# Optimization experiments

Hardware: AMD Instinct MI355X
Metric: run time of the kernel (lower is better)

## Reference

```python
import jax, jax.numpy as jnp
import numpy as np

IMC = 256
EPS = 1e-6
BN_EPS = 1e-5
GRID = (69.12, 79.36)      # (depth, width) in meters
OFF = (0.0, -39.68, 0.0)   # (xoff, yoff, zoff)
RES = 0.64
ZMIN, ZMAX = -3.0, 2.76
SCALES = [0.25, 0.125, 0.0625, 0.03125, 0.015625]


def make_corners():
    # replicates make_grid(): corner lattice in lidar coords, shape [nz, nx, ny, 3]
    nx = int(round(GRID[0] / RES)) + 1   # 109
    ny = int(round(GRID[1] / RES)) + 1   # 125
    nz = int(round((ZMAX - ZMIN) / RES)) + 1  # 10
    xc = RES * np.arange(nx) + OFF[0]
    yc = GRID[1] - RES * np.arange(ny) + OFF[1]
    zc = ZMAX - RES * np.arange(nz)
    xx, yy = np.meshgrid(xc, yc, indexing='ij')
    base = np.stack([xx, yy, np.full_like(xx, OFF[2])], axis=-1)  # [nx,ny,3]
    zoffs = np.stack([np.zeros(nz), np.zeros(nz), zc], axis=-1)   # [nz,3]
    corners = base[None] + zoffs[:, None, None, :]
    return jnp.asarray(corners, jnp.float32)


def grid_sample(img, grid):
    # img [B,C,H,W]; grid [B,P,N,2] xy in [-1,1]; bilinear, zero padding, align_corners=False
    B, C, H, W = img.shape
    x = (grid[..., 0] + 1.0) * (W * 0.5) - 0.5
    y = (grid[..., 1] + 1.0) * (H * 0.5) - 0.5
    x0f = jnp.floor(x); y0f = jnp.floor(y)
    wx = (x - x0f).reshape(B, 1, -1)
    wy = (y - y0f).reshape(B, 1, -1)
    x0 = x0f.astype(jnp.int32); y0 = y0f.astype(jnp.int32)
    flat = img.reshape(B, C, H * W)
    def g(xi, yi):
        ok = ((xi >= 0) & (xi < W) & (yi >= 0) & (yi < H)).reshape(B, 1, -1)
        idx = (jnp.clip(yi, 0, H - 1) * W + jnp.clip(xi, 0, W - 1)).reshape(B, 1, -1)
        return jnp.take_along_axis(flat, idx, axis=2) * ok
    v00 = g(x0, y0); v01 = g(x0 + 1, y0); v10 = g(x0, y0 + 1); v11 = g(x0 + 1, y0 + 1)
    out = (v00 * (1 - wx) + v01 * wx) * (1 - wy) + (v10 * (1 - wx) + v11 * wx) * wy
    return out.reshape(B, C, grid.shape[1], grid.shape[2])


def oft(feats, calib, corners, scale, w, b):
    B, C, Hf, Wf = feats.shape
    # perspective projection of grid corners into the image plane
    hom = jnp.einsum('bij,zdwj->bzdwi', calib[:, :, :3], corners) + calib[:, None, None, None, :, 3]
    xy = hom[..., :2] / hom[..., 2:3]                      # [B,nz,nx,ny,2]
    img_size = jnp.array([Wf, Hf], jnp.float32) / scale
    nc = jnp.clip(2.0 * xy / img_size - 1.0, -1.0, 1.0)
    mn = jnp.minimum(nc[:, :-1, :-1, :-1], nc[:, :-1, 1:, :-1])
    mx = jnp.maximum(nc[:, 1:, 1:, 1:], nc[:, 1:, :-1, 1:])
    bbox = jnp.concatenate([mn, mx], axis=-1)              # [B,Zc,Dc,Wc,4]
    _, Zc, Dc, Wc, _ = bbox.shape
    bbox = bbox.reshape(B, Zc, Dc * Wc, 4)
    area = ((bbox[..., 2] - bbox[..., 0]) * (bbox[..., 3] - bbox[..., 1])
            * (Hf * Wf * 0.25) + EPS)[:, None]             # [B,1,Zc,N]
    visible = (area > EPS).astype(feats.dtype)
    ii = jnp.cumsum(jnp.cumsum(feats, axis=-1), axis=-2)   # integral image
    tl = grid_sample(ii, jnp.stack([bbox[..., 0], bbox[..., 1]], -1))
    br = grid_sample(ii, jnp.stack([bbox[..., 2], bbox[..., 3]], -1))
    tr = grid_sample(ii, jnp.stack([bbox[..., 2], bbox[..., 1]], -1))
    bl = grid_sample(ii, jnp.stack([bbox[..., 0], bbox[..., 3]], -1))
    vox = (tl + br - tr - bl) / area * visible             # [B,C,Zc,N]
    vox = vox.transpose(0, 3, 1, 2).reshape(B * Dc * Wc, C * Zc)
    ortho = jax.nn.relu(vox @ w.T + b).reshape(B, Dc, Wc, -1)
    return ortho.transpose(0, 3, 2, 1)                     # [B,imc,Wc,Dc]


def attention(x, aw, ab):
    s = jax.nn.sigmoid(x.mean(axis=(2, 3)) @ aw.T + ab)
    return x * s[:, :, None, None]


def conv3x3(x, w, stride):
    return jax.lax.conv_general_dilated(x, w, (stride, stride), ((1, 1), (1, 1)),
                                        dimension_numbers=('NCHW', 'OIHW', 'NCHW'))


def bn(x, g, b, m, v):
    scale = g / jnp.sqrt(v + BN_EPS)
    return (x - m[None, :, None, None]) * scale[None, :, None, None] + b[None, :, None, None]


def make_calib(B):
    K = np.array([[560.0, 0.0, 640.0], [0.0, 560.0, 192.0], [0.0, 0.0, 1.0]])
    Rt = np.array([[0.0, -1.0, 0.0, 0.05],   # lidar(x fwd, y left, z up) -> cam(x right, y down, z fwd)
                   [0.0, 0.0, -1.0, -0.30],
                   [1.0, 0.0, 0.0, 0.27]])
    P = K @ Rt
    return jnp.asarray(np.tile(P[None], (B, 1, 1)), jnp.float32)


def setup_inputs() -> dict:
    key = jax.random.key(0)
    ks = jax.random.split(key, 16)
    B = 1
    shapes = [(B, IMC, 96, 320), (B, IMC, 48, 160), (B, IMC, 24, 80), (B, IMC, 12, 40), (B, IMC, 6, 20)]
    feats = [jax.random.normal(ks[i], s, jnp.float32) * 0.1 for i, s in enumerate(shapes)]
    HC = 9 * IMC  # height_channels = int((2.76-(-3))/0.64 * 256) = 2304
    inp = {
        'feats04': feats[0], 'feats08': feats[1], 'feats16': feats[2],
        'feats32': feats[3], 'feats64': feats[4],
        'calib': make_calib(B),
        'oft_w': jax.random.normal(ks[5], (5, IMC, HC), jnp.float32) * 0.02,
        'oft_b': jax.random.normal(ks[6], (5, IMC), jnp.float32) * 0.02,
        'att_w': jax.random.normal(ks[7], (IMC, IMC), jnp.float32) * 0.05,
        'att_b': jnp.zeros((IMC,), jnp.float32),
        'conv1_w': jax.random.normal(ks[8], (IMC, IMC * 5, 3, 3), jnp.float32) * 0.02,
        'bn1_g': 1.0 + 0.1 * jax.random.normal(ks[9], (IMC,), jnp.float32),
        'bn1_b': 0.05 * jax.random.normal(ks[10], (IMC,), jnp.float32),
        'bn1_m': 0.05 * jax.random.normal(ks[11], (IMC,), jnp.float32),
        'bn1_v': jax.random.uniform(ks[12], (IMC,), jnp.float32, 0.5, 1.5),
        'conv2_w': jax.random.normal(ks[13], (IMC, IMC, 3, 3), jnp.float32) * 0.02,
        'bn2_g': 1.0 + 0.1 * jax.random.normal(ks[14], (IMC,), jnp.float32),
        'bn2_b': jnp.zeros((IMC,), jnp.float32),
        'bn2_m': jnp.zeros((IMC,), jnp.float32),
        'bn2_v': jax.random.uniform(ks[15], (IMC,), jnp.float32, 0.5, 1.5),
    }
    return inp


def reference(feats04, feats08, feats16, feats32, feats64, calib,
              oft_w, oft_b, att_w, att_b,
              conv1_w, bn1_g, bn1_b, bn1_m, bn1_v,
              conv2_w, bn2_g, bn2_b, bn2_m, bn2_v):
    corners = make_corners()
    feats = [feats04, feats08, feats16, feats32, feats64]
    orthos = [attention(oft(f, calib, corners, s, oft_w[i], oft_b[i]), att_w, att_b)
              for i, (f, s) in enumerate(zip(feats, SCALES))]
    x = jnp.concatenate(orthos, axis=1)            # [B, 5*imc, 124, 108]
    x = jax.nn.relu(bn(conv3x3(x, conv1_w, 2), bn1_g, bn1_b, bn1_m, bn1_v))
    x = jax.nn.relu(bn(conv3x3(x, conv2_w, 1), bn2_g, bn2_b, bn2_m, bn2_v))
    return x                                       # [B, imc, 62, 54]
```

## Files before the change

kernel.cpp:

```cpp
#include <hip/hip_runtime.h>

typedef __attribute__((ext_vector_type(8))) short short8;
typedef __attribute__((ext_vector_type(4))) float float4v;
typedef __attribute__((ext_vector_type(4))) int int4v;
typedef __attribute__((ext_vector_type(4))) unsigned short ushort4v;

#define NBOX 13392
#define ZC 9
#define KOFT 2304
#define NPIX 3348
#define NBLK0 105
#define NBLKC 27
#define TILEK 4096
#define NBSTRIDE 294912
#define VOXSZ 30965760
#define TAPINTS 16

__device__ __forceinline__ unsigned short f2bf(float f) {
  union { float f; unsigned int i; } v; v.f = f;
  unsigned int r = v.i + 0x7FFFu + ((v.i >> 16) & 1u);
  return (unsigned short)(r >> 16);
}
__device__ __forceinline__ float bf2f(unsigned short u) {
  union { unsigned int i; float f; } v; v.i = ((unsigned int)u) << 16; return v.f;
}
__device__ __forceinline__ float i2f(int i) {
  union { int i; float f; } v; v.i = i; return v.f;
}

__device__ __constant__ int cHFs[5] = {96, 48, 24, 12, 6};
__device__ __constant__ int cWFs[5] = {320, 160, 80, 40, 20};
__device__ __constant__ size_t cIIof[5] = {0, 7864320, 9830400, 10321920, 10444800};

__device__ __forceinline__ const int* uniform_ptr(const int* p) {
  unsigned lo = (unsigned)(uintptr_t)p;
  unsigned hi = (unsigned)((uintptr_t)p >> 32);
  lo = (unsigned)__builtin_amdgcn_readfirstlane((int)lo);
  hi = (unsigned)__builtin_amdgcn_readfirstlane((int)hi);
  return (const int*)(((uintptr_t)hi << 32) | (uintptr_t)lo);
}

__device__ __forceinline__ void async16(const unsigned short* g, unsigned short* l) {
  __builtin_amdgcn_global_load_lds(
      (const __attribute__((address_space(1))) unsigned int*)g,
      (__attribute__((address_space(3))) unsigned int*)l, 16, 0, 0);
}

__global__ void k_alpha_beta(const float* __restrict__ oft_b,
                             const float* __restrict__ g1, const float* __restrict__ b1,
                             const float* __restrict__ m1, const float* __restrict__ v1,
                             const float* __restrict__ g2, const float* __restrict__ b2,
                             const float* __restrict__ m2, const float* __restrict__ v2,
                             float* __restrict__ ALPHA, float* __restrict__ BETA,
                             float* __restrict__ MEANS, unsigned short* __restrict__ ZPAGE) {
  int g = blockIdx.x, c = threadIdx.x;
  float al, be;
  if (g < 5) { al = 1.f; be = oft_b[g * 256 + c]; MEANS[g * 256 + c] = 0.f; }
  else {
    const float* gg = (g == 5) ? g1 : g2;
    const float* bb = (g == 5) ? b1 : b2;
    const float* mm = (g == 5) ? m1 : m2;
    const float* vv = (g == 5) ? v1 : v2;
    al = gg[c] / sqrtf(vv[c] + 1e-5f);
    be = bb[c] - mm[c] * al;
  }
  ALPHA[g * 256 + c] = al; BETA[g * 256 + c] = be;
  if (g == 0) ZPAGE[c] = 0;
}

__global__ void k_wpermT(const float* __restrict__ w, unsigned short* __restrict__ wp) {
  int b = blockIdx.x;
  int sc = b >> 8, oc = b & 255;
  int t = threadIdx.x;
  const float* src = w + (size_t)b * 2304;
  int row = oc & 127, cb = oc >> 7;
  unsigned short* dst = wp + (size_t)sc * 589824 + (size_t)cb * 294912 + row * 8;
#pragma unroll
  for (int i = 0; i < 9; ++i) {
    int idx = i * 256 + t;
    float v = src[idx];
    int c = idx / 9, z = idx - c * 9;
    int k = z * 256 + c;
    int s = k >> 5, kc = (k >> 3) & 3, j = k & 7;
    dst[(size_t)s * 4096 + kc * 1024 + j] = f2bf(v);
  }
}

__global__ void k_wperm1T(const float* __restrict__ w, const float* __restrict__ satt,
                          unsigned short* __restrict__ wp) {
  int oc = blockIdx.x;
  int t = threadIdx.x;
  const float* src = w + (size_t)oc * 11520;
  int row = oc & 127, cb = oc >> 7;
  unsigned short* dst = wp + (size_t)cb * (9 * 40 * 4096) + row * 8;
#pragma unroll
  for (int i = 0; i < 45; ++i) {
    int idx = i * 256 + t;
    float v = src[idx];
    int ic = idx / 9, r = idx - ic * 9;
    int s = ic >> 5, kc = (ic >> 3) & 3, j = ic & 7;
    dst[(size_t)(r * 40 + s) * 4096 + kc * 1024 + j] = f2bf(v * satt[ic]);
  }
}

__global__ void k_wperm2T(const float* __restrict__ w, unsigned short* __restrict__ wp) {
  int oc = blockIdx.x;
  int t = threadIdx.x;
  const float* src = w + (size_t)oc * 2304;
  int row = oc & 127, cb = oc >> 7;
  unsigned short* dst = wp + (size_t)cb * (9 * 8 * 4096) + row * 8;
#pragma unroll
  for (int i = 0; i < 9; ++i) {
    int idx = i * 256 + t;
    float v = src[idx];
    int ic = idx / 9, r = idx - ic * 9;
    int s = ic >> 5, kc = (ic >> 3) & 3, j = ic & 7;
    dst[(size_t)(r * 8 + s) * 4096 + kc * 1024 + j] = f2bf(v);
  }
}

__global__ void k_tapsA(const float* __restrict__ calib, int* __restrict__ taps, int s0) {
  int idx = blockIdx.x * 256 + threadIdx.x;
  if (idx >= ZC * NBOX) return;
  int slab = blockIdx.y, sc = s0 + slab;
  int Hf = cHFs[sc], Wf = cWFs[sc];
  float areaScale = (float)(Hf * Wf) * 0.25f;
  int z = idx / NBOX, n = idx % NBOX;
  int d = n / 124, wj = n % 124;
  float P[12];
#pragma unroll
  for (int i = 0; i < 12; ++i) P[i] = calib[i];
  auto proj = [&](int k, int i, int j, float& nxo, float& nyo) {
    float X = 0.64f * (float)i;
    float Y = 39.68f - 0.64f * (float)j;
    float Z = 2.76f - 0.64f * (float)k;
    float hx = P[0] * X + P[1] * Y + P[2]  * Z + P[3];
    float hy = P[4] * X + P[5] * Y + P[6]  * Z + P[7];
    float hz = P[8] * X + P[9] * Y + P[10] * Z + P[11];
    float px = hx / hz, py = hy / hz;
    nxo = 2.f * px / 1280.f - 1.f; nxo = fminf(fmaxf(nxo, -1.f), 1.f);
    nyo = 2.f * py / 384.f  - 1.f; nyo = fminf(fmaxf(nyo, -1.f), 1.f);
  };
  float ax, ay, bx, by, cx, cy, dx, dy;
  proj(z,     d,     wj,     ax, ay);
  proj(z,     d + 1, wj,     bx, by);
  proj(z + 1, d + 1, wj + 1, cx, cy);
  proj(z + 1, d,     wj + 1, dx, dy);
  float x0 = fminf(ax, bx), y0 = fminf(ay, by);
  float x1 = fmaxf(cx, dx), y1 = fmaxf(cy, dy);
  float rawA = (x1 - x0) * (y1 - y0) * areaScale;
  int* ob = taps + (size_t)slab * (ZC * NBOX * TAPINTS) + (size_t)idx * TAPINTS;
  if (!(rawA > 0.f)) { ob[0] = 0; return; }
  float inv = 1.f / (rawA + 1e-6f);

  float u0 = (x0 + 1.f) * ((float)Wf * 0.5f) - 0.5f;
  float u1 = (x1 + 1.f) * ((float)Wf * 0.5f) - 0.5f;
  float fu0 = floorf(u0), fu1 = floorf(u1);
  int cx0 = (int)fu0, cx1 = (int)fu1;
  float wx0 = u0 - fu0, wx1 = u1 - fu1;
  int xs[4]; float xw[4];
  xs[0] = cx0; xs[1] = cx0 + 1; xs[2] = cx1; xs[3] = cx1 + 1;
  xw[0] = (1.f - wx0) * inv; xw[1] = wx0 * inv;
  xw[2] = -(1.f - wx1) * inv; xw[3] = -wx1 * inv;
  int dcx = cx1 - cx0;
  if (dcx == 0)      { xw[0] += xw[2]; xw[1] += xw[3]; xw[2] = 0.f; xw[3] = 0.f; }
  else if (dcx == 1) { xw[1] += xw[2]; xw[2] = xw[3]; xs[2] = xs[3]; xw[3] = 0.f; }
#pragma unroll
  for (int j = 0; j < 4; ++j) {
    if (xs[j] < 0 || xs[j] >= Wf) xw[j] = 0.f;
    xs[j] = min(max(xs[j], 0), Wf - 1);
  }
#define CSWX(a, b) { if (xw[a] == 0.f && xw[b] != 0.f) { \
    float tw = xw[a]; xw[a] = xw[b]; xw[b] = tw; \
    int ts = xs[a]; xs[a] = xs[b]; xs[b] = ts; } }
  CSWX(0, 1) CSWX(2, 3) CSWX(0, 2) CSWX(1, 3) CSWX(1, 2)
#undef CSWX
  int nx = (xw[0] != 0.f) + (xw[1] != 0.f) + (xw[2] != 0.f) + (xw[3] != 0.f);

  float v0 = (y0 + 1.f) * ((float)Hf * 0.5f) - 0.5f;
  float v1 = (y1 + 1.f) * ((float)Hf * 0.5f) - 0.5f;
  float fv0 = floorf(v0), fv1 = floorf(v1);
  int ry0 = (int)fv0, ry1 = (int)fv1;
  float wy0 = v0 - fv0, wy1 = v1 - fv1;
  int ys[4]; float yw[4];
  ys[0] = ry0; ys[1] = ry0 + 1; ys[2] = ry1; ys[3] = ry1 + 1;
  yw[0] = 1.f - wy0; yw[1] = wy0; yw[2] = -(1.f - wy1); yw[3] = -wy1;
  int dcy = ry1 - ry0;
  if (dcy == 0)      { yw[0] += yw[2]; yw[1] += yw[3]; yw[2] = 0.f; yw[3] = 0.f; }
  else if (dcy == 1) { yw[1] += yw[2]; yw[2] = yw[3]; ys[2] = ys[3]; yw[3] = 0.f; }
#pragma unroll
  for (int j = 0; j < 4; ++j) {
    if (ys[j] < 0 || ys[j] >= Hf) yw[j] = 0.f;
    ys[j] = min(max(ys[j], 0), Hf - 1);
  }
#define CSWY(a, b) { if (yw[a] == 0.f && yw[b] != 0.f) { \
    float tw = yw[a]; yw[a] = yw[b]; yw[b] = tw; \
    int ts = ys[a]; ys[a] = ys[b]; ys[b] = ts; } }
  CSWY(0, 1) CSWY(2, 3) CSWY(0, 2) CSWY(1, 3) CSWY(1, 2)
#undef CSWY
  int ny = (yw[0] != 0.f) + (yw[1] != 0.f) + (yw[2] != 0.f) + (yw[3] != 0.f);

  if (nx == 0 || ny == 0) { ob[0] = 0; return; }

  int4v* obv = (int4v*)ob;
  obv[0] = (int4v){(xs[0] << 10) | (nx << 25) | (ny << 28),
                   xs[1] << 10, xs[2] << 10, xs[3] << 10};
  obv[1] = (int4v){ys[0] * Wf * 1024, ys[1] * Wf * 1024,
                   ys[2] * Wf * 1024, ys[3] * Wf * 1024};
  float4v* wb = (float4v*)ob;
  wb[2] = (float4v){xw[0], xw[1], xw[2], xw[3]};
  wb[3] = (float4v){yw[0], yw[1], yw[2], yw[3]};
}

__global__ void k_transpose_all(const float* __restrict__ f0, const float* __restrict__ f1,
                                const float* __restrict__ f2, const float* __restrict__ f3,
                                const float* __restrict__ f4, float* __restrict__ II) {
  int b = blockIdx.x;
  int sc, cx;
  if (b < 480)      { sc = 0; cx = b; }
  else if (b < 600) { sc = 1; cx = b - 480; }
  else if (b < 630) { sc = 2; cx = b - 600; }
  else if (b < 638) { sc = 3; cx = b - 630; }
  else              { sc = 4; cx = b - 638; }
  const int Ss[5] = {30720, 7680, 1920, 480, 120};
  const float* srcs[5] = {f0, f1, f2, f3, f4};
  int S = Ss[sc];
  const float* src = srcs[sc];
  float* dst = II + cIIof[sc];
  __shared__ float tile[64][65];
  int t = threadIdx.x;
  int wave = t >> 6, lane = t & 63;
  int s0 = cx * 64, c0 = blockIdx.y * 64;
#pragma unroll
  for (int i = 0; i < 16; ++i) {
    int c_l = wave * 16 + i;
    if (s0 + lane < S) tile[c_l][lane] = src[(size_t)(c0 + c_l) * S + s0 + lane];
  }
  __syncthreads();
#pragma unroll
  for (int i = 0; i < 16; ++i) {
    int s_l = wave * 16 + i;
    if (s0 + s_l < S) dst[(size_t)(s0 + s_l) * 256 + c0 + lane] = tile[lane][s_l];
  }
}

__global__ void k_cumw_all(float* __restrict__ II) {
  int b = blockIdx.x;
  int sc, h;
  if (b < 96)       { sc = 0; h = b; }
  else if (b < 144) { sc = 1; h = b - 96; }
  else if (b < 168) { sc = 2; h = b - 144; }
  else if (b < 180) { sc = 3; h = b - 168; }
  else              { sc = 4; h = b - 180; }
  int Wf = cWFs[sc];
  float* p = II + cIIof[sc] + (size_t)h * Wf * 256 + threadIdx.x;
  float acc = 0.f;
#pragma unroll 4
  for (int w = 0; w < Wf; ++w) { acc += p[(size_t)w * 256]; p[(size_t)w * 256] = acc; }
}

__global__ void k_cumh_all(float* __restrict__ II) {
  int b = blockIdx.x;
  int sc, w;
  if (b < 320)      { sc = 0; w = b; }
  else if (b < 480) { sc = 1; w = b - 320; }
  else if (b < 560) { sc = 2; w = b - 480; }
  else if (b < 600) { sc = 3; w = b - 560; }
  else              { sc = 4; w = b - 600; }
  const int Hfs[5] = {96, 48, 24, 12, 6};
  int Hf = Hfs[sc];
  size_t stride = (size_t)cWFs[sc] * 256;
  float* p = II + cIIof[sc] + (size_t)w * 256 + threadIdx.x;
  float acc = 0.f;
#pragma unroll 4
  for (int h = 0; h < Hf; ++h) { acc += p[h * stride]; p[h * stride] = acc; }
}

__global__ __launch_bounds__(512) void k_sampleA(const float* __restrict__ II,
                                                 const int* __restrict__ taps,
                                                 unsigned short* __restrict__ voxT,
                                                 int s0) {
  __shared__ unsigned short st[3][8][66][4];
  int t = threadIdx.x;
  int wave = t >> 6, lane = t & 63;
  int n = blockIdx.x * 8 + wave;
  int zg = blockIdx.y * 3;
  int slab = blockIdx.z, sc = s0 + slab;
  const float* ii = II + cIIof[sc];
  const int* tbase = taps + (size_t)slab * (ZC * NBOX * TAPINTS);
  unsigned short* vox = voxT + (size_t)slab * VOXSZ;
  const char* iib = (const char*)ii + (lane << 4);
#pragma unroll
  for (int dz = 0; dz < 3; ++dz) {
    int z = zg + dz;
    const int* tb = uniform_ptr(tbase + (size_t)(z * NBOX + n) * TAPINTS);
    int xo[4], yo[4]; float xw[4], yw[4];
#pragma unroll
    for (int i = 0; i < 4; ++i) xo[i] = tb[i];
#pragma unroll
    for (int i = 0; i < 4; ++i) yo[i] = tb[4 + i];
#pragma unroll
    for (int i = 0; i < 4; ++i) xw[i] = i2f(tb[8 + i]);
#pragma unroll
    for (int i = 0; i < 4; ++i) yw[i] = i2f(tb[12 + i]);
    unsigned h = (unsigned)xo[0];
    int nx = (h >> 25) & 7;
    int ny = (h >> 28) & 7;
    xo[0] = (int)(h & 0x01FFFFFFu);
    ushort4v o;
    if (ny == 0) {
      o[0] = 0; o[1] = 0; o[2] = 0; o[3] = 0;
    } else {
      int o_[16]; float w_[16];
#pragma unroll
      for (int r = 0; r < 4; ++r)
#pragma unroll
        for (int c = 0; c < 4; ++c) {
          o_[r * 4 + c] = yo[r] + xo[c];
          w_[r * 4 + c] = yw[r] * xw[c];
        }
      float4v a0 = {0.f, 0.f, 0.f, 0.f}, a1 = a0;
#define TAP(i, acc) { float4v t_ = *(const float4v*)(iib + (size_t)(unsigned)o_[i]); acc += t_ * w_[i]; }
      TAP(0, a0)
      if (nx > 1) TAP(1, a1)
      if (nx > 2) TAP(2, a0)
      if (nx > 3) TAP(3, a1)
      if (ny > 1) {
        TAP(4, a0)
        if (nx > 1) TAP(5, a1)
        if (nx > 2) TAP(6, a0)
        if (nx > 3) TAP(7, a1)
      }
      if (ny > 2) {
        TAP(8, a0)
        if (nx > 1) TAP(9, a1)
        if (nx > 2) TAP(10, a0)
        if (nx > 3) TAP(11, a1)
      }
      if (ny > 3) {
        TAP(12, a0)
        if (nx > 1) TAP(13, a1)
        if (nx > 2) TAP(14, a0)
        if (nx > 3) TAP(15, a1)
      }
#undef TAP
      float4v acc = a0 + a1;
#pragma unroll
      for (int j = 0; j < 4; ++j) o[j] = f2bf(acc[j]);
    }
    *(ushort4v*)&st[dz][wave][lane][0] = o;
  }
  __syncthreads();
  int nb = (blockIdx.x * 8) >> 7;
  int r0 = (blockIdx.x * 8) & 127;
  unsigned short* outb = vox + (size_t)nb * NBSTRIDE + (size_t)r0 * 32;
  int lane32 = t & 31;
  int row = lane32 >> 2, kc = lane32 & 3;
#pragma unroll
  for (int p = 0; p < 2; ++p) {
    int q = p * 16 + (t >> 5);
    if (q < 24) {
      int zq = q >> 3;
      int si = q & 7;
      short8 v = *(const short8*)&st[zq][row][si * 8 + kc * 2][0];
      *(short8*)(outb + (size_t)(zg + zq) * 32768 + (size_t)si * 4096
                 + (size_t)(row * 32 + kc * 8)) = v;
    }
  }
}

__global__ __launch_bounds__(512) void k_gemmT_all(
    const unsigned short* __restrict__ AT, const unsigned short* __restrict__ BT,
    const float* __restrict__ beta, unsigned short* __restrict__ xbuf,
    float* __restrict__ means, int s0) {
  __shared__ unsigned short ls[8704];
  __shared__ float lsm[128];
  unsigned short* lsA = ls;
  unsigned short* lsB = ls + 4096;
  int t = threadIdx.x;
  int lane = t & 63, wave = t >> 6;
  int l15 = lane & 15, quad = lane >> 4;
  int nb = blockIdx.x, cb = blockIdx.y;
  int slab = blockIdx.z, sc = s0 + slab;
  int wrow = (wave & 3) * 32, wcol = (wave >> 2) * 64;

  const unsigned short* ga = AT + (size_t)slab * VOXSZ + (size_t)nb * NBSTRIDE + t * 8;
  const unsigned short* gb = BT + (size_t)sc * 589824 + (size_t)cb * NBSTRIDE + t * 8;
  unsigned short* ldA = lsA + t * 8;
  unsigned short* ldB = lsB + t * 8;

  float4v acc[2][4];
#pragma unroll
  for (int mi = 0; mi < 2; ++mi)
#pragma unroll
    for (int ni = 0; ni < 4; ++ni) acc[mi][ni] = (float4v){0.f, 0.f, 0.f, 0.f};

  for (int s = 0; s < 72; ++s) {
    async16(ga, ldA);
    async16(gb, ldB);
    ga += TILEK; gb += TILEK;
    __syncthreads();
    short8 af[2], bf[4];
    const short8* pA = (const short8*)lsA;
    const short8* pB = (const short8*)lsB;
#pragma unroll
    for (int mi = 0; mi < 2; ++mi) af[mi] = pA[(wrow + mi * 16 + l15) * 4 + quad];
#pragma unroll
    for (int ni = 0; ni < 4; ++ni) bf[ni] = pB[quad * 128 + wcol + ni * 16 + l15];
#pragma unroll
    for (int mi = 0; mi < 2; ++mi)
#pragma unroll
      for (int ni = 0; ni < 4; ++ni)
        acc[mi][ni] = __builtin_amdgcn_mfma_f32_16x16x32_bf16(af[mi], bf[ni], acc[mi][ni], 0, 0, 0);
    __syncthreads();
  }

  float bval[4];
  float msum[4] = {0.f, 0.f, 0.f, 0.f};
#pragma unroll
  for (int ni = 0; ni < 4; ++ni)
    bval[ni] = beta[sc * 256 + cb * 128 + wcol + ni * 16 + l15];
#pragma unroll
  for (int ph = 0; ph < 2; ++ph) {
    if ((wrow >> 6) == ph) {
#pragma unroll
      for (int mi = 0; mi < 2; ++mi)
#pragma unroll
        for (int ni = 0; ni < 4; ++ni)
#pragma unroll
          for (int j = 0; j < 4; ++j) {
            int row = (wrow & 63) + mi * 16 + quad * 4 + j;
            int col = wcol + ni * 16 + l15;
            float v = acc[mi][ni][j] + bval[ni];
            v = v > 0.f ? v : 0.f;
            ls[row * 136 + col] = f2bf(v);
            if (nb * 128 + ph * 64 + row < NBOX) msum[ni] += v;
          }
    }
    __syncthreads();
#pragma unroll
    for (int it = 0; it < 2; ++it) {
      int idx = it * 512 + t;
      int row = idx >> 4, ch = idx & 15;
      int nn = nb * 128 + ph * 64 + row;
      if (nn < NBOX) {
        short8 v = *(const short8*)&ls[row * 136 + ch * 8];
        *(short8*)(xbuf + (size_t)nn * 1280 + sc * 256 + cb * 128 + ch * 8) = v;
      }
    }
    __syncthreads();
  }
  if (t < 128) lsm[t] = 0.f;
  __syncthreads();
#pragma unroll
  for (int ni = 0; ni < 4; ++ni)
    atomicAdd(&lsm[wcol + ni * 16 + l15], msum[ni]);
  __syncthreads();
  if (t < 128) atomicAdd(&means[sc * 256 + cb * 128 + t], lsm[t]);
}

__global__ __launch_bounds__(256) void k_gemmT(
    const unsigned short* __restrict__ AT, const unsigned short* __restrict__ BT,
    float* __restrict__ part) {
  __shared__ unsigned short lsA[4096];
  __shared__ unsigned short lsB[4096];
  int t = threadIdx.x;
  int lane = t & 63, wave = t >> 6;
  int l15 = lane & 15, quad = lane >> 4;
  int nb = blockIdx.x, cb = blockIdx.y, ks = blockIdx.z;
  int wrow = (wave >> 1) * 64, wcol = (wave & 1) * 64;

  const unsigned short* ga = AT + (size_t)nb * NBSTRIDE + (size_t)ks * 18 * TILEK + t * 8;
  const unsigned short* gb = BT + (size_t)cb * NBSTRIDE + (size_t)ks * 18 * TILEK + t * 8;
  unsigned short* ldA = lsA + t * 8;
  unsigned short* ldB = lsB + t * 8;

  float4v acc[4][4];
#pragma unroll
  for (int mi = 0; mi < 4; ++mi)
#pragma unroll
    for (int ni = 0; ni < 4; ++ni) acc[mi][ni] = (float4v){0.f, 0.f, 0.f, 0.f};

  for (int s = 0; s < 18; ++s) {
    async16(ga, ldA);
    async16(ga + 2048, ldA + 2048);
    async16(gb, ldB);
    async16(gb + 2048, ldB + 2048);
    ga += TILEK; gb += TILEK;
    __syncthreads();
    short8 af[4], bf[4];
    const short8* pA = (const short8*)lsA;
    const short8* pB = (const short8*)lsB;
#pragma unroll
    for (int mi = 0; mi < 4; ++mi) af[mi] = pA[(wrow + mi * 16 + l15) * 4 + quad];
#pragma unroll
    for (int ni = 0; ni < 4; ++ni) bf[ni] = pB[quad * 128 + wcol + ni * 16 + l15];
#pragma unroll
    for (int mi = 0; mi < 4; ++mi)
#pragma unroll
      for (int ni = 0; ni < 4; ++ni)
        acc[mi][ni] = __builtin_amdgcn_mfma_f32_16x16x32_bf16(af[mi], bf[ni], acc[mi][ni], 0, 0, 0);
    __syncthreads();
  }

#pragma unroll
  for (int mi = 0; mi < 4; ++mi) {
    int nb0 = nb * 128 + wrow + mi * 16 + quad * 4;
#pragma unroll
    for (int j = 0; j < 4; ++j) {
      int nn = nb0 + j;
      if (nn < NBOX) {
#pragma unroll
        for (int ni = 0; ni < 4; ++ni) {
          int oc = cb * 128 + wcol + ni * 16 + l15;
          part[((size_t)ks * NBOX + nn) * 256 + oc] = acc[mi][ni][j];
        }
      }
    }
  }
}

__global__ void k_redoft(const float* __restrict__ part, const float* __restrict__ beta,
                         unsigned short* __restrict__ xbuf, int choff) {
  int n = blockIdx.x, oc = threadIdx.x;
  float v = part[(size_t)n * 256 + oc]
          + part[((size_t)NBOX + n) * 256 + oc]
          + part[((size_t)2 * NBOX + n) * 256 + oc]
          + part[((size_t)3 * NBOX + n) * 256 + oc];
  v += beta[oc];
  v = v > 0.f ? v : 0.f;
  xbuf[(size_t)n * 1280 + choff + oc] = f2bf(v);
}

template <int MODE>
__global__ __launch_bounds__(512) void k_gemmS(
    const unsigned short* __restrict__ A, const unsigned short* __restrict__ BT,
    float* __restrict__ part, const unsigned short* __restrict__ zpage) {
  constexpr int KIC   = (MODE == 1) ? 1280 : 256;
  constexpr int STEPS = KIC / 32;
  __shared__ unsigned short lsA[4096];
  __shared__ unsigned short lsB[4096];
  int t = threadIdx.x;
  int lane = t & 63, wave = t >> 6;
  int l15 = lane & 15, quad = lane >> 4;
  int n0 = blockIdx.x * 128, oc0 = blockIdx.y * 128;
  int r = blockIdx.z;
  int wrow = (wave & 3) * 32, wcol = (wave >> 2) * 64;
  int srow = t & 127, skc = t >> 7;

  int p = n0 + srow;
  int oy = p / 54, ox = p - oy * 54;
  int ky = r / 3, kx = r - ky * 3;
  bool valid; int sp;
  if (MODE == 1) {
    int ih = 2 * oy + ky - 1, iw = 2 * ox + kx - 1;
    valid = (p < NPIX) && ((unsigned)ih < 124u) && ((unsigned)iw < 108u);
    sp = iw * 124 + ih;
  } else {
    int ih = oy + ky - 1, iw = ox + kx - 1;
    valid = (p < NPIX) && ((unsigned)ih < 62u) && ((unsigned)iw < 54u);
    sp = ih * 54 + iw;
  }
  const unsigned short* ga = valid ? (A + (size_t)sp * KIC + skc * 8) : zpage;
  int astep = valid ? 32 : 0;
  const unsigned short* gb = BT + ((size_t)(blockIdx.y * 9 + r) * STEPS) * TILEK + t * 8;
  unsigned short* ldA = lsA + t * 8;
  unsigned short* ldB = lsB + t * 8;

  float4v acc[2][4];
#pragma unroll
  for (int mi = 0; mi < 2; ++mi)
#pragma unroll
    for (int ni = 0; ni < 4; ++ni) acc[mi][ni] = (float4v){0.f, 0.f, 0.f, 0.f};

  for (int s = 0; s < STEPS; ++s) {
    async16(ga, ldA);
    async16(gb, ldB);
    ga += astep; gb += TILEK;
    __syncthreads();
    short8 af[2], bf[4];
    const short8* pA = (const short8*)lsA;
    const short8* pB = (const short8*)lsB;
#pragma unroll
    for (int mi = 0; mi < 2; ++mi) af[mi] = pA[quad * 128 + wrow + mi * 16 + l15];
#pragma unroll
    for (int ni = 0; ni < 4; ++ni) bf[ni] = pB[quad * 128 + wcol + ni * 16 + l15];
#pragma unroll
    for (int mi = 0; mi < 2; ++mi)
#pragma unroll
      for (int ni = 0; ni < 4; ++ni)
        acc[mi][ni] = __builtin_amdgcn_mfma_f32_16x16x32_bf16(af[mi], bf[ni], acc[mi][ni], 0, 0, 0);
    __syncthreads();
  }

#pragma unroll
  for (int mi = 0; mi < 2; ++mi) {
    int nb0 = n0 + wrow + mi * 16 + quad * 4;
#pragma unroll
    for (int j = 0; j < 4; ++j) {
      int nn = nb0 + j;
      if (nn < NPIX) {
#pragma unroll
        for (int ni = 0; ni < 4; ++ni) {
          int oc = oc0 + wcol + ni * 16 + l15;
          part[((size_t)r * NPIX + nn) * 256 + oc] = acc[mi][ni][j];
        }
      }
    }
  }
}

template <bool F32OUT>
__global__ void k_redconv(const float* __restrict__ part, const float* __restrict__ alpha,
                          const float* __restrict__ beta, void* __restrict__ outv) {
  int p = blockIdx.x, oc = threadIdx.x;
  float v = 0.f;
#pragma unroll
  for (int r = 0; r < 9; ++r) v += part[((size_t)r * NPIX + p) * 256 + oc];
  v = v * alpha[oc] + beta[oc];
  v = v > 0.f ? v : 0.f;
  if (F32OUT) ((float*)outv)[(size_t)oc * NPIX + p] = v;
  else ((unsigned short*)outv)[(size_t)p * 256 + oc] = f2bf(v);
}

__global__ void k_means2(const unsigned short* __restrict__ x, float* __restrict__ means) {
  int tid = threadIdx.x;
  if (tid >= 160) return;
  int c0 = tid * 8;
  int r0 = blockIdx.x * 64;
  float part[8] = {0.f, 0.f, 0.f, 0.f, 0.f, 0.f, 0.f, 0.f};
  for (int i = 0; i < 64; ++i) {
    int row = r0 + i;
    if (row < NBOX) {
      short8 v = *(const short8*)(x + (size_t)row * 1280 + c0);
#pragma unroll
      for (int j = 0; j < 8; ++j) part[j] += bf2f((unsigned short)v[j]);
    }
  }
#pragma unroll
  for (int j = 0; j < 8; ++j) atomicAdd(&means[c0 + j], part[j]);
}

__global__ void k_att(const float* __restrict__ means, const float* __restrict__ aw,
                      const float* __restrict__ ab, float* __restrict__ satt) {
  int sc = blockIdx.x, c = threadIdx.x;
  __shared__ float m[256];
  m[c] = means[sc * 256 + c] * (1.f / (float)NBOX);
  __syncthreads();
  float acc = ab[c];
  for (int j = 0; j < 256; ++j) acc += m[j] * aw[c * 256 + j];
  satt[sc * 256 + c] = 1.f / (1.f + expf(-acc));
}

extern "C" void kernel_launch(void* const* d_in, const int* in_sizes, int n_in,
                              void* d_out, int out_size, void* d_ws, size_t ws_size,
                              hipStream_t stream) {
  const float* feats[5];
  for (int i = 0; i < 5; ++i) feats[i] = (const float*)d_in[i];
  const float* calib   = (const float*)d_in[5];
  const float* oft_w   = (const float*)d_in[6];
  const float* oft_b   = (const float*)d_in[7];
  const float* att_w   = (const float*)d_in[8];
  const float* att_b   = (const float*)d_in[9];
  const float* conv1_w = (const float*)d_in[10];
  const float* bn1g = (const float*)d_in[11];
  const float* bn1b = (const float*)d_in[12];
  const float* bn1m = (const float*)d_in[13];
  const float* bn1v = (const float*)d_in[14];
  const float* conv2_w = (const float*)d_in[15];
  const float* bn2g = (const float*)d_in[16];
  const float* bn2b = (const float*)d_in[17];
  const float* bn2m = (const float*)d_in[18];
  const float* bn2v = (const float*)d_in[19];

  char* ws = (char*)d_ws;
  size_t off = 0;
  auto alloc = [&](size_t bytes) -> void* {
    void* p = ws + off; off += (bytes + 255) & ~(size_t)255; return p;
  };
  unsigned short* WPERMT = (unsigned short*)alloc((size_t)5 * 589824 * 2);
  unsigned short* WC1T   = (unsigned short*)alloc((size_t)2949120 * 2);
  unsigned short* WC2T   = (unsigned short*)alloc((size_t)589824 * 2);
  float*          II     = (float*)alloc((size_t)10475520 * 4);
  unsigned short* XBUF   = (unsigned short*)alloc((size_t)NBOX * 1280 * 2);
  unsigned short* Y1     = (unsigned short*)alloc((size_t)NPIX * 256 * 2);
  float*          MEANS  = (float*)alloc(1280 * 4);
  float*          SATT   = (float*)alloc(1280 * 4);
  float*          ALPHA  = (float*)alloc(7 * 256 * 4);
  float*          BETA   = (float*)alloc(7 * 256 * 4);
  unsigned short* ZPAGE  = (unsigned short*)alloc(256 * 2);

  const size_t SLAB    = (size_t)VOXSZ * 2;
  const size_t TAPSZ_C = (size_t)ZC * NBOX * 64;
  const size_t PARTSZ  = (size_t)4 * NBOX * 256 * 4;
  size_t rem = (ws_size > off) ? ws_size - off : 0;

  int NS, NT;
  int* TAPS; unsigned short* VOXT; float* PART;
  if (rem >= 2 * SLAB + 5 * TAPSZ_C) {
    NT = 5;
    TAPS = (int*)alloc(5 * TAPSZ_C);
    NS = (int)((rem - 5 * TAPSZ_C) / SLAB); if (NS > 5) NS = 5;
    VOXT = (unsigned short*)alloc((size_t)NS * SLAB);
    PART = (float*)VOXT;
  } else if (rem >= 2 * (SLAB + TAPSZ_C)) {
    NT = 0;
    NS = (int)(rem / (SLAB + TAPSZ_C)); if (NS > 5) NS = 5;
    TAPS = (int*)alloc((size_t)NS * TAPSZ_C);
    VOXT = (unsigned short*)alloc((size_t)NS * SLAB);
    PART = (float*)VOXT;
  } else {
    NS = 0; NT = 0;
    VOXT = (unsigned short*)alloc(SLAB);
    PART = (float*)alloc(PARTSZ);
    TAPS = (int*)PART;
  }
  (void)in_sizes; (void)n_in; (void)out_size;

  k_alpha_beta<<<7, 256, 0, stream>>>(oft_b, bn1g, bn1b, bn1m, bn1v,
                                      bn2g, bn2b, bn2m, bn2v, ALPHA, BETA, MEANS, ZPAGE);
  k_wpermT<<<1280, 256, 0, stream>>>(oft_w, WPERMT);
  k_wperm2T<<<256, 256, 0, stream>>>(conv2_w, WC2T);

  k_transpose_all<<<dim3(640, 4), 256, 0, stream>>>(feats[0], feats[1], feats[2],
                                                    feats[3], feats[4], II);
  k_cumw_all<<<186, 256, 0, stream>>>(II);
  k_cumh_all<<<620, 256, 0, stream>>>(II);

  const int TGRID = (ZC * NBOX + 255) / 256;
  if (NS > 0) {
    if (NT == 5)
      k_tapsA<<<dim3(TGRID, 5), 256, 0, stream>>>(calib, TAPS, 0);
    int g0 = 0;
    while (g0 < 5) {
      int gsz = 5 - g0; if (gsz > NS) gsz = NS;
      int* tg = TAPS;
      if (NT == 5) tg = TAPS + (size_t)g0 * (ZC * NBOX * TAPINTS);
      else k_tapsA<<<dim3(TGRID, gsz), 256, 0, stream>>>(calib, TAPS, g0);
      k_sampleA<<<dim3(NBOX / 8, 3, gsz), 512, 0, stream>>>(II, tg, VOXT, g0);
      k_gemmT_all<<<dim3(NBLK0, 2, gsz), 512, 0, stream>>>(VOXT, WPERMT, BETA,
                                                           XBUF, MEANS, g0);
      g0 += gsz;
    }
  } else {
    for (int s = 0; s < 5; ++s) {
      k_tapsA<<<dim3(TGRID, 1), 256, 0, stream>>>(calib, TAPS, s);
      k_sampleA<<<dim3(NBOX / 8, 3, 1), 512, 0, stream>>>(II, TAPS, VOXT, s);
      k_gemmT<<<dim3(NBLK0, 2, 4), 256, 0, stream>>>(
          VOXT, WPERMT + (size_t)s * 589824, PART);
      k_redoft<<<NBOX, 256, 0, stream>>>(PART, BETA + s * 256, XBUF, s * 256);
    }
    k_means2<<<(NBOX + 63) / 64, 256, 0, stream>>>(XBUF, MEANS);
  }

  k_att<<<5, 256, 0, stream>>>(MEANS, att_w, att_b, SATT);
  k_wperm1T<<<256, 256, 0, stream>>>(conv1_w, SATT, WC1T);

  k_gemmS<1><<<dim3(NBLKC, 2, 9), 512, 0, stream>>>(XBUF, WC1T, PART, ZPAGE);
  k_redconv<false><<<NPIX, 256, 0, stream>>>(PART, ALPHA + 5 * 256, BETA + 5 * 256, Y1);

  k_gemmS<2><<<dim3(NBLKC, 2, 9), 512, 0, stream>>>(Y1, WC2T, PART, ZPAGE);
  k_redconv<true><<<NPIX, 256, 0, stream>>>(PART, ALPHA + 6 * 256, BETA + 6 * 256, d_out);
}
```

Measured before the change: 738.0 us.

## Double-buffer LDS tiles in GEMM kernels and hoist tap loads in sampler

Both the transposed OFT GEMM and the strided conv GEMM now use two LDS buffers. The next K-tile's async global-to-LDS copy is issued before the MFMAs run on the current tile, and the barrier that used to follow each load is gone, so memory latency can overlap with compute. The sampling kernel first loads tap descriptors for all three z-levels, then runs the gather loops, so the uniform scalar loads can be in flight together. The trade-off is a larger LDS footprint (32KB per block), which may lower occupancy, plus more live registers in the sampler.

```diff
diff --git a/kernel.cpp b/kernel.cpp
--- a/kernel.cpp
+++ b/kernel.cpp
@@ -290,23 +290,26 @@
   const int* tbase = taps + (size_t)slab * (ZC * NBOX * TAPINTS);
   unsigned short* vox = voxT + (size_t)slab * VOXSZ;
   const char* iib = (const char*)ii + (lane << 4);
+
+  int xo3[3][4], yo3[3][4], xwi[3][4], ywi[3][4];
 #pragma unroll
   for (int dz = 0; dz < 3; ++dz) {
-    int z = zg + dz;
-    const int* tb = uniform_ptr(tbase + (size_t)(z * NBOX + n) * TAPINTS);
-    int xo[4], yo[4]; float xw[4], yw[4];
-#pragma unroll
-    for (int i = 0; i < 4; ++i) xo[i] = tb[i];
-#pragma unroll
-    for (int i = 0; i < 4; ++i) yo[i] = tb[4 + i];
-#pragma unroll
-    for (int i = 0; i < 4; ++i) xw[i] = i2f(tb[8 + i]);
-#pragma unroll
-    for (int i = 0; i < 4; ++i) yw[i] = i2f(tb[12 + i]);
-    unsigned h = (unsigned)xo[0];
+    const int* tb = uniform_ptr(tbase + (size_t)((zg + dz) * NBOX + n) * TAPINTS);
+#pragma unroll
+    for (int i = 0; i < 4; ++i) xo3[dz][i] = tb[i];
+#pragma unroll
+    for (int i = 0; i < 4; ++i) yo3[dz][i] = tb[4 + i];
+#pragma unroll
+    for (int i = 0; i < 4; ++i) xwi[dz][i] = tb[8 + i];
+#pragma unroll
+    for (int i = 0; i < 4; ++i) ywi[dz][i] = tb[12 + i];
+  }
+#pragma unroll
+  for (int dz = 0; dz < 3; ++dz) {
+    unsigned h = (unsigned)xo3[dz][0];
     int nx = (h >> 25) & 7;
     int ny = (h >> 28) & 7;
-    xo[0] = (int)(h & 0x01FFFFFFu);
+    int xo0 = (int)(h & 0x01FFFFFFu);
     ushort4v o;
     if (ny == 0) {
       o[0] = 0; o[1] = 0; o[2] = 0; o[3] = 0;
@@ -316,8 +319,9 @@
       for (int r = 0; r < 4; ++r)
 #pragma unroll
         for (int c = 0; c < 4; ++c) {
-          o_[r * 4 + c] = yo[r] + xo[c];
-          w_[r * 4 + c] = yw[r] * xw[c];
+          int xoc = (c == 0) ? xo0 : xo3[dz][c];
+          o_[r * 4 + c] = yo3[dz][r] + xoc;
+          w_[r * 4 + c] = i2f(ywi[dz][r]) * i2f(xwi[dz][c]);
         }
       float4v a0 = {0.f, 0.f, 0.f, 0.f}, a1 = a0;
 #define TAP(i, acc) { float4v t_ = *(const float4v*)(iib + (size_t)(unsigned)o_[i]); acc += t_ * w_[i]; }
@@ -373,10 +377,8 @@
     const unsigned short* __restrict__ AT, const unsigned short* __restrict__ BT,
     const float* __restrict__ beta, unsigned short* __restrict__ xbuf,
     float* __restrict__ means, int s0) {
-  __shared__ unsigned short ls[8704];
+  __shared__ unsigned short ls[16384];
   __shared__ float lsm[128];
-  unsigned short* lsA = ls;
-  unsigned short* lsB = ls + 4096;
   int t = threadIdx.x;
   int lane = t & 63, wave = t >> 6;
   int l15 = lane & 15, quad = lane >> 4;
@@ -386,8 +388,6 @@
 
   const unsigned short* ga = AT + (size_t)slab * VOXSZ + (size_t)nb * NBSTRIDE + t * 8;
   const unsigned short* gb = BT + (size_t)sc * 589824 + (size_t)cb * NBSTRIDE + t * 8;
-  unsigned short* ldA = lsA + t * 8;
-  unsigned short* ldB = lsB + t * 8;
 
   float4v acc[2][4];
 #pragma unroll
@@ -395,14 +395,22 @@
 #pragma unroll
     for (int ni = 0; ni < 4; ++ni) acc[mi][ni] = (float4v){0.f, 0.f, 0.f, 0.f};
 
+  async16(ga, ls + t * 8);
+  async16(gb, ls + 4096 + t * 8);
+  ga += TILEK; gb += TILEK;
+  __syncthreads();
+
   for (int s = 0; s < 72; ++s) {
-    async16(ga, ldA);
-    async16(gb, ldB);
-    ga += TILEK; gb += TILEK;
-    __syncthreads();
+    unsigned short* buf = ls + (s & 1) * 8192;
+    if (s < 71) {
+      unsigned short* nbuf = ls + ((s + 1) & 1) * 8192;
+      async16(ga, nbuf + t * 8);
+      async16(gb, nbuf + 4096 + t * 8);
+      ga += TILEK; gb += TILEK;
+    }
     short8 af[2], bf[4];
-    const short8* pA = (const short8*)lsA;
-    const short8* pB = (const short8*)lsB;
+    const short8* pA = (const short8*)buf;
+    const short8* pB = (const short8*)(buf + 4096);
 #pragma unroll
     for (int mi = 0; mi < 2; ++mi) af[mi] = pA[(wrow + mi * 16 + l15) * 4 + quad];
 #pragma unroll
@@ -538,8 +546,7 @@
     float* __restrict__ part, const unsigned short* __restrict__ zpage) {
   constexpr int KIC   = (MODE == 1) ? 1280 : 256;
   constexpr int STEPS = KIC / 32;
-  __shared__ unsigned short lsA[4096];
-  __shared__ unsigned short lsB[4096];
+  __shared__ unsigned short ls[16384];
   int t = threadIdx.x;
   int lane = t & 63, wave = t >> 6;
   int l15 = lane & 15, quad = lane >> 4;
@@ -564,8 +571,6 @@
   const unsigned short* ga = valid ? (A + (size_t)sp * KIC + skc * 8) : zpage;
   int astep = valid ? 32 : 0;
   const unsigned short* gb = BT + ((size_t)(blockIdx.y * 9 + r) * STEPS) * TILEK + t * 8;
-  unsigned short* ldA = lsA + t * 8;
-  unsigned short* ldB = lsB + t * 8;
 
   float4v acc[2][4];
 #pragma unroll
@@ -573,14 +578,22 @@
 #pragma unroll
     for (int ni = 0; ni < 4; ++ni) acc[mi][ni] = (float4v){0.f, 0.f, 0.f, 0.f};
 
+  async16(ga, ls + t * 8);
+  async16(gb, ls + 4096 + t * 8);
+  ga += astep; gb += TILEK;
+  __syncthreads();
+
   for (int s = 0; s < STEPS; ++s) {
-    async16(ga, ldA);
-    async16(gb, ldB);
-    ga += astep; gb += TILEK;
-    __syncthreads();
+    unsigned short* buf = ls + (s & 1) * 8192;
+    if (s < STEPS - 1) {
+      unsigned short* nbuf = ls + ((s + 1) & 1) * 8192;
+      async16(ga, nbuf + t * 8);
+      async16(gb, nbuf + 4096 + t * 8);
+      ga += astep; gb += TILEK;
+    }
     short8 af[2], bf[4];
-    const short8* pA = (const short8*)lsA;
-    const short8* pB = (const short8*)lsB;
+    const short8* pA = (const short8*)buf;
+    const short8* pB = (const short8*)(buf + 4096);
 #pragma unroll
     for (int mi = 0; mi < 2; ++mi) af[mi] = pA[quad * 128 + wrow + mi * 16 + l15];
 #pragma unroll
```

After: 744.7 us. No clear change (+0.9%).
